# Kernel tuning notes

Hardware: AMD Instinct MI355X
Metric: run time of the kernel (lower is better)

Reference implementation:

```python
import jax, jax.numpy as jnp
import numpy as np

# Module constants (from init_kwargs)
MAP_BBOX = (-5.0, -5.0, 5.0, 5.0)  # h1, w1, h2, w2
V_BBOX = (0.0, 3.0)
MAP_RES = (64, 64)
V_RES = 8
XYZ_TO_H, XYZ_TO_W, XYZ_TO_V = 0, 1, 2
SCALE = 4
PCN_H = 64


def mish(x):
    return x * jnp.tanh(jax.nn.softplus(x))


def conv_d2(x, w):
    # 3x3 conv, dilation 2, padding 2, stride 1, no bias (NCHW / OIHW)
    return jax.lax.conv_general_dilated(
        x, w, window_strides=(1, 1), padding=((2, 2), (2, 2)),
        rhs_dilation=(2, 2), dimension_numbers=('NCHW', 'OIHW', 'NCHW'))


def maxpool3s2(x):
    # MaxPool2d(kernel=3, stride=2, padding=1); torch pads with -inf
    return jax.lax.reduce_window(
        x, -jnp.inf, jax.lax.max,
        window_dimensions=(1, 1, 3, 3), window_strides=(1, 1, 2, 2),
        padding=((0, 0), (0, 0), (1, 1), (1, 1)))


def setup_inputs() -> dict:
    key = jax.random.key(0)
    k1, k2, k3, k4, k5 = jax.random.split(key, 5)
    N, H, W = 64, 256, 256
    B = 8
    return {
        'rgb': jax.random.normal(k1, (N, 3, H, W), dtype=jnp.float32),
        'surf_xyz': jax.random.normal(k2, (N, 3, H, W), dtype=jnp.float32),
        'W1': jax.random.normal(k3, (PCN_H, 3, 3, 3), dtype=jnp.float32) * 0.1,
        'W2': jax.random.normal(k4, (PCN_H, PCN_H, 3, 3), dtype=jnp.float32) * 0.05,
        'index': jax.random.randint(k5, (N,), 0, B, dtype=jnp.int32),
        'batch_size': B,
    }


def reference(rgb, surf_xyz, W1, W2, index, batch_size):
    N, _, H, W = surf_xyz.shape
    s = SCALE
    Hs, Ws = H // s, W // s

    # avg_pool2d(rgb, 4)
    surf_rgb = rgb.reshape(N, 3, Hs, s, Ws, s).mean(axis=(3, 5))
    # subsampled xyz: surf_xyz[:, :, 2::4, 2::4]
    sxyz = surf_xyz[:, :, s // 2::s, s // 2::s]  # (N,3,Hs,Ws)
    _index = jnp.broadcast_to(index[:, None, None], (N, Hs, Ws))

    # rgb_conv_net: conv -> mish -> maxpool -> conv -> mish -> maxpool (dropout=0)
    feat = maxpool3s2(mish(conv_d2(rgb, W1)))
    feat = maxpool3s2(mish(conv_d2(feat, W2)))  # (N, h, Hs, Ws)

    # flatten  (valid_points is None path)
    hdim = feat.shape[1]
    flat_features = feat.transpose(0, 2, 3, 1).reshape(-1, hdim)   # (M, h)
    flat_xyz = sxyz.transpose(0, 2, 3, 1).reshape(-1, 3)           # (M, 3)
    flat_rgb = surf_rgb.transpose(0, 2, 3, 1).reshape(-1, 3)       # (M, 3)
    flat_index = _index.reshape(-1)                                # (M,)

    # coord_to_grid (float->int cast truncates toward zero, matching torch .long())
    map_h, map_w = MAP_RES
    h1, w1, h2, w2 = MAP_BBOX
    v1, v2 = V_BBOX
    hs = ((flat_xyz[:, XYZ_TO_H] - h1) * map_h / (h2 - h1)).astype(jnp.int32)
    ws = ((flat_xyz[:, XYZ_TO_W] - w1) * map_w / (w2 - w1)).astype(jnp.int32)
    vs = ((flat_xyz[:, XYZ_TO_V] - v1) * V_RES / (v2 - v1)).astype(jnp.int32)
    valid = ((hs >= 0) & (hs < map_h) & (ws >= 0) & (ws < map_w)
             & (vs >= 0) & (vs < V_RES))

    B, V = batch_size, V_RES
    P = B * V * map_h * map_w
    lin = ((flat_index * V + vs) * map_h + hs) * map_w + ws
    # route invalid points to a dummy segment that gets dropped
    lin_safe = jnp.where(valid, lin, P)

    sums = jax.ops.segment_sum(flat_features, lin_safe, num_segments=P + 1)[:P]
    rgbs = jax.ops.segment_sum(flat_rgb, lin_safe, num_segments=P + 1)[:P]
    counts = jax.ops.segment_sum(
        jnp.ones_like(lin_safe), lin_safe, num_segments=P + 1)[:P]

    feature_map = sums.reshape(B, V, map_h, map_w, hdim).transpose(0, 4, 1, 2, 3)
    rgb_map = rgbs.reshape(B, V, map_h, map_w, 3).transpose(0, 4, 1, 2, 3)
    feature_counts = counts.reshape(B, V, map_h, map_w)[:, None]
    return feature_map, feature_counts, rgb_map
```

## Files before the change

### kernel.cpp

```cpp
#include <hip/hip_runtime.h>
#include <hip/hip_bf16.h>
#include <math.h>

#define N_IMG 64
#define CH    64
#define F1_R  136
#define F1_C  136
#define F1_IMG_STRIDE ((size_t)F1_R * F1_C * 64)
#define F1_ROW_STRIDE (F1_C * 64)
#define FEAT1_BYTES ((size_t)N_IMG * F1_IMG_STRIDE * 2)

#define OUT_CNT_BASE 16777216
#define OUT_RGB_BASE 17039360

typedef short bf16x8 __attribute__((ext_vector_type(8)));
typedef float f32x4  __attribute__((ext_vector_type(4)));

__device__ __forceinline__ float fast_mish(float x) {
    float xc = fminf(x, 20.0f);
    float t  = __expf(xc);
    float n  = t * (t + 2.0f);
    float y  = x * n / (n + 2.0f);
    return (x > 20.0f) ? x : y;
}

__device__ __forceinline__ unsigned short f2bf(float f) {
    unsigned u = __float_as_uint(f);
    unsigned r = (u + 0x7FFFu + ((u >> 16) & 1u)) >> 16;
    return (unsigned short)r;
}

__global__ __launch_bounds__(256) void point_kernel(
    const float* __restrict__ rgb,
    const float* __restrict__ sxyz,
    const int*   __restrict__ index,
    float*       __restrict__ out,
    int*         __restrict__ lin_pt)
{
    int p = blockIdx.x * 256 + threadIdx.x;
    int n  = p >> 12;
    int r  = p & 4095;
    int hs = r >> 6;
    int ws = r & 63;

    int row = hs * 4 + 2, col = ws * 4 + 2;
    const float* sx = sxyz + (size_t)n * 3 * 65536;
    float X = sx[row * 256 + col];
    float Y = sx[65536 + row * 256 + col];
    float Z = sx[2 * 65536 + row * 256 + col];

    int hb = (int)(((X + 5.0f) * 64.0f) / 10.0f);
    int wb = (int)(((Y + 5.0f) * 64.0f) / 10.0f);
    int vb = (int)((Z * 8.0f) / 3.0f);
    bool valid = (hb >= 0) & (hb < 64) & (wb >= 0) & (wb < 64) & (vb >= 0) & (vb < 8);

    int b   = index[n];
    int lin = ((b * 8 + vb) * 64 + hb) * 64 + wb;
    lin_pt[p] = valid ? lin : -1;

    if (valid) {
        atomicAdd(out + OUT_CNT_BASE + lin, 1.0f);
        int rem = lin & 32767;
        #pragma unroll
        for (int c = 0; c < 3; c++) {
            const float* rg = rgb + (size_t)(n * 3 + c) * 65536;
            float s = 0.0f;
            #pragma unroll
            for (int i = 0; i < 4; i++)
                #pragma unroll
                for (int j = 0; j < 4; j++)
                    s += rg[(hs * 4 + i) * 256 + (ws * 4 + j)];
            atomicAdd(out + OUT_RGB_BASE + b * 98304 + c * 32768 + rem, s * 0.0625f);
        }
    }
}

__global__ __launch_bounds__(1024) void conv1_mfma_kernel(
    const float* __restrict__ rgb,
    const float* __restrict__ w1,
    __hip_bfloat16* __restrict__ feat1)
{
    int b2 = ((blockIdx.x & 7) << 9) + (blockIdx.x >> 3);
    const int n  = b2 >> 6;
    const int pr = b2 & 63;
    const int tid  = threadIdx.x;
    const int lane = tid & 63;
    const int w    = tid >> 6;

    __shared__ __align__(16) char smem[81920];
    unsigned short* wlds = (unsigned short*)smem;
    unsigned short* in_t = (unsigned short*)(smem + 4096);

    for (int i = tid; i < 2048; i += 1024) {
        int co = i >> 5, k = i & 31;
        wlds[i] = (k < 27) ? f2bf(w1[co * 27 + k]) : (unsigned short)0;
    }
    {
        const float* img = rgb + (size_t)n * 3 * 65536;
        for (int i = tid; i < 7144; i += 1024) {
            unsigned short v = 0;
            if (i < 7128) {
                int ci  = i / 2376;
                int rem = i - ci * 2376;
                int rr  = rem / 264;
                int cc  = rem - rr * 264;
                int gy  = 4 * pr - 3 + rr;
                int gx  = cc - 2;
                if (gy >= 0 && gy < 256 && gx >= 0 && gx < 256)
                    v = f2bf(img[ci * 65536 + gy * 256 + gx]);
            }
            in_t[i] = v;
        }
    }
    __syncthreads();

    int boff[8];
    #pragma unroll
    for (int j = 0; j < 8; j++) {
        int k = ((lane >> 4) << 3) + j;
        if (k < 27) {
            int ci = k / 9, t = k - 9 * ci, ky = t / 3, kx = t - 3 * ky;
            boff[j] = (ci * 2376 + 2 * ky * 264 + 2 * kx + (lane & 15)) * 2;
        } else {
            boff[j] = 7128 * 2;
        }
    }

    bf16x8 a[4];
    #pragma unroll
    for (int mt = 0; mt < 4; mt++)
        a[mt] = *reinterpret_cast<const bf16x8*>(
            wlds + (mt * 16 + (lane & 15)) * 32 + ((lane >> 4) << 3));

    f32x4 acc[5][4];
    #pragma unroll
    for (int tt = 0; tt < 5; tt++)
        #pragma unroll
        for (int mt = 0; mt < 4; mt++)
            acc[tt][mt] = (f32x4){0.f, 0.f, 0.f, 0.f};

    const char* in_b = (const char*)in_t;
    #pragma unroll
    for (int tt = 0; tt < 5; tt++) {
        int t5 = w * 5 + tt;
        int r  = t5 >> 4;
        int x0 = (t5 & 15) << 4;
        int base = (r * 264 + x0) * 2;
        unsigned short e[8];
        #pragma unroll
        for (int j = 0; j < 8; j++)
            e[j] = *reinterpret_cast<const unsigned short*>(in_b + base + boff[j]);
        bf16x8 b;
        #pragma unroll
        for (int j = 0; j < 8; j++) b[j] = (short)e[j];
        #pragma unroll
        for (int mt = 0; mt < 4; mt++)
            acc[tt][mt] = __builtin_amdgcn_mfma_f32_16x16x32_bf16(a[mt], b, acc[tt][mt], 0, 0, 0);
    }

    __syncthreads();

    unsigned short* pool = (unsigned short*)smem;
    const int ybase = 4 * pr - 1;

    #pragma unroll
    for (int p = 0; p < 2; p++) {
        #pragma unroll
        for (int tt = 0; tt < 5; tt++) {
            int t5 = w * 5 + tt;
            int r  = t5 >> 4;
            int x  = ((t5 & 15) << 4) + (lane & 15);
            bool dead = (ybase + r) < 0;
            #pragma unroll
            for (int m2 = 0; m2 < 2; m2++) {
                int mt  = p * 2 + m2;
                int col = m2 * 16 + ((lane >> 4) << 2);
                unsigned long long pk = 0;
                #pragma unroll
                for (int q = 0; q < 4; q++) {
                    float v = dead ? -INFINITY : fast_mish(acc[tt][mt][q]);
                    pk |= (unsigned long long)f2bf(v) << (16 * q);
                }
                int byte = (((r * 256 + x) * 32) + col) * 2;
                byte ^= (x & 7) << 4;
                *reinterpret_cast<unsigned long long*>((char*)pool + byte) = pk;
            }
        }
        __syncthreads();
        for (int i = tid; i < 8192; i += 1024) {
            int pp = i >> 12;
            int c  = (i >> 5) & 127;
            int cl = i & 31;
            float m = -INFINITY;
            #pragma unroll
            for (int dy = 0; dy < 3; dy++) {
                int lr = 2 * pp + dy;
                #pragma unroll
                for (int dx = 0; dx < 3; dx++) {
                    int x = 2 * c - 1 + dx;
                    if (x < 0) continue;
                    int byte = ((((lr * 256) + x) * 32) + cl) * 2;
                    byte ^= (x & 7) << 4;
                    unsigned short hv = *reinterpret_cast<const unsigned short*>((char*)pool + byte);
                    m = fmaxf(m, __uint_as_float((unsigned)hv << 16));
                }
            }
            unsigned short* dst = (unsigned short*)(feat1 + (size_t)n * F1_IMG_STRIDE
                + (size_t)(2 * pr + pp + 4) * F1_ROW_STRIDE + (size_t)(c + 4) * 64 + p * 32 + cl);
            *dst = f2bf(m);
        }
        __syncthreads();
    }
}

__global__ __launch_bounds__(640, 3) void conv2_mfma_kernel(
    const __hip_bfloat16* __restrict__ feat1,
    const float* __restrict__ w2,
    const int*   __restrict__ lin_pt,
    float*       __restrict__ out)
{
    int b2 = ((blockIdx.x & 7) << 8) + (blockIdx.x >> 3);
    const int n  = b2 >> 5;
    const int pr = b2 & 31;
    const int tid  = threadIdx.x;
    const int lane = tid & 63;
    const int w    = tid >> 6;
    const int lrow = w >> 1;
    const int chalf = w & 1;
    const int y = 4 * pr - 1 + lrow;

    __shared__ __align__(16) char smem[81920];

    for (int i = tid; i < 36864; i += 640) {
        int t  = i >> 12;
        int co = (i >> 6) & 63;
        int ci = i & 63;
        unsigned short h = f2bf(w2[(co * 64 + ci) * 9 + t]);
        int byte = ((((t << 6) + co) << 6) + ci) << 1;
        byte ^= (co & 7) << 4;
        *reinterpret_cast<unsigned short*>(smem + byte) = h;
    }
    __syncthreads();

    f32x4 acc[4][4];
    #pragma unroll
    for (int mt = 0; mt < 4; mt++)
        #pragma unroll
        for (int nt = 0; nt < 4; nt++)
            acc[mt][nt] = (f32x4){0.f, 0.f, 0.f, 0.f};

    const __hip_bfloat16* bbase = feat1 + (size_t)n * F1_IMG_STRIDE
        + ((size_t)(y + 2) * F1_C + (lane & 15) + chalf * 64 + 2) * 64
        + ((lane >> 4) << 3);

    #pragma unroll
    for (int ky = 0; ky < 3; ky++) {
        #pragma unroll
        for (int kx = 0; kx < 3; kx++) {
            const int t = ky * 3 + kx;
            #pragma unroll
            for (int s = 0; s < 2; s++) {
                bf16x8 a[4];
                #pragma unroll
                for (int mt = 0; mt < 4; mt++) {
                    int co = mt * 16 + (lane & 15);
                    int byte = ((((t << 6) + co) << 6) + (s << 5) + ((lane >> 4) << 3)) << 1;
                    byte ^= (co & 7) << 4;
                    a[mt] = *reinterpret_cast<const bf16x8*>(smem + byte);
                }
                const __hip_bfloat16* bp = bbase + (ky * 2 * F1_C + kx * 2) * 64 + s * 32;
                #pragma unroll
                for (int nt = 0; nt < 4; nt++) {
                    bf16x8 b = *reinterpret_cast<const bf16x8*>(bp + nt * 1024);
                    #pragma unroll
                    for (int mt = 0; mt < 4; mt++)
                        acc[mt][nt] = __builtin_amdgcn_mfma_f32_16x16x32_bf16(
                            a[mt], b, acc[mt][nt], 0, 0, 0);
                }
            }
        }
    }

    __syncthreads();

    const bool deadrow = (y < 0);
    #pragma unroll
    for (int nt = 0; nt < 4; nt++) {
        int col = chalf * 64 + nt * 16 + (lane & 15);
        #pragma unroll
        for (int mt = 0; mt < 4; mt++) {
            int co0 = mt * 16 + ((lane >> 4) << 2);
            unsigned long long pk = 0;
            #pragma unroll
            for (int r4 = 0; r4 < 4; r4++) {
                float v = deadrow ? -INFINITY : fast_mish(acc[mt][nt][r4]);
                pk |= (unsigned long long)f2bf(v) << (16 * r4);
            }
            int byte = ((((lrow * 128 + col) << 6) + co0) << 1);
            byte ^= (col & 7) << 4;
            *reinterpret_cast<unsigned long long*>(smem + byte) = pk;
        }
    }
    __syncthreads();

    const int pbase = (n << 12) + ((pr << 1) << 6);
    for (int i = tid; i < 8192; i += 640) {
        int pp = i >> 12;
        int c  = (i >> 6) & 63;
        int co = i & 63;
        float m = -INFINITY;
        #pragma unroll
        for (int dy = 0; dy < 3; dy++) {
            int lr = 2 * pp + dy;
            #pragma unroll
            for (int dx = 0; dx < 3; dx++) {
                int x = 2 * c - 1 + dx;
                if (x < 0 || x > 127) continue;
                int byte = ((((lr * 128 + x) << 6) + co) << 1) ^ ((x & 7) << 4);
                unsigned short hv = *reinterpret_cast<const unsigned short*>(smem + byte);
                m = fmaxf(m, __uint_as_float((unsigned)hv << 16));
            }
        }
        int lin = lin_pt[pbase + (pp << 6) + c];
        if (lin >= 0)
            atomicAdd(out + (size_t)(lin >> 15) * 2097152 + (size_t)co * 32768 + (lin & 32767), m);
    }
}

extern "C" void kernel_launch(void* const* d_in, const int* in_sizes, int n_in,
                              void* d_out, int out_size, void* d_ws, size_t ws_size,
                              hipStream_t stream)
{
    const float* rgb   = (const float*)d_in[0];
    const float* sxyz  = (const float*)d_in[1];
    const float* w1    = (const float*)d_in[2];
    const float* w2    = (const float*)d_in[3];
    const int*   index = (const int*)d_in[4];
    float* out = (float*)d_out;

    __hip_bfloat16* feat1 = (__hip_bfloat16*)d_ws;
    int* lin_pt = (int*)((char*)d_ws + FEAT1_BYTES);

    hipMemsetAsync(d_out, 0, (size_t)out_size * 4, stream);
    hipMemsetAsync(d_ws, 0, FEAT1_BYTES, stream);

    point_kernel<<<1024, 256, 0, stream>>>(rgb, sxyz, index, out, lin_pt);
    conv1_mfma_kernel<<<4096, 1024, 0, stream>>>(rgb, w1, feat1);
    conv2_mfma_kernel<<<2048, 640, 0, stream>>>(feat1, w2, lin_pt, out);
}
```

Baseline: 1.211 ms.

## Pre-convert conv2 weights to bf16 in global memory and halve conv2 LDS footprint

Adds a small kernel that converts W2 to bf16 once into workspace, so conv2 blocks no longer each convert and stage the full weight tensor in LDS. A-fragments are read directly from global/L2, and the mish+maxpool epilogue is split into two 32-channel passes so shared memory drops from 80 KB to 40 KB. The smaller LDS allows more resident blocks per CU and removes the per-block weight prologue. The cost is more global/L2 traffic for weight loads inside the MFMA loop, an extra sync, and one extra kernel launch.

```diff
diff --git a/kernel.cpp b/kernel.cpp
--- a/kernel.cpp
+++ b/kernel.cpp
@@ -9,6 +9,7 @@
 #define F1_IMG_STRIDE ((size_t)F1_R * F1_C * 64)
 #define F1_ROW_STRIDE (F1_C * 64)
 #define FEAT1_BYTES ((size_t)N_IMG * F1_IMG_STRIDE * 2)
+#define LINPT_BYTES (262144 * 4)
 
 #define OUT_CNT_BASE 16777216
 #define OUT_RGB_BASE 17039360
@@ -28,6 +29,18 @@
     unsigned u = __float_as_uint(f);
     unsigned r = (u + 0x7FFFu + ((u >> 16) & 1u)) >> 16;
     return (unsigned short)r;
+}
+
+__global__ __launch_bounds__(256) void w2cvt_kernel(
+    const float* __restrict__ w2, unsigned short* __restrict__ w2bf)
+{
+    int i = blockIdx.x * 256 + threadIdx.x;
+    if (i < 36864) {
+        int t  = i >> 12;
+        int co = (i >> 6) & 63;
+        int ci = i & 63;
+        w2bf[i] = f2bf(w2[(co * 64 + ci) * 9 + t]);
+    }
 }
 
 __global__ __launch_bounds__(256) void point_kernel(
@@ -213,9 +226,9 @@
     }
 }
 
-__global__ __launch_bounds__(640, 3) void conv2_mfma_kernel(
+__global__ __launch_bounds__(640) void conv2_mfma_kernel(
     const __hip_bfloat16* __restrict__ feat1,
-    const float* __restrict__ w2,
+    const unsigned short* __restrict__ w2bf,
     const int*   __restrict__ lin_pt,
     float*       __restrict__ out)
 {
@@ -229,18 +242,7 @@
     const int chalf = w & 1;
     const int y = 4 * pr - 1 + lrow;
 
-    __shared__ __align__(16) char smem[81920];
-
-    for (int i = tid; i < 36864; i += 640) {
-        int t  = i >> 12;
-        int co = (i >> 6) & 63;
-        int ci = i & 63;
-        unsigned short h = f2bf(w2[(co * 64 + ci) * 9 + t]);
-        int byte = ((((t << 6) + co) << 6) + ci) << 1;
-        byte ^= (co & 7) << 4;
-        *reinterpret_cast<unsigned short*>(smem + byte) = h;
-    }
-    __syncthreads();
+    __shared__ __align__(16) char smem[40960];
 
     f32x4 acc[4][4];
     #pragma unroll
@@ -252,6 +254,7 @@
     const __hip_bfloat16* bbase = feat1 + (size_t)n * F1_IMG_STRIDE
         + ((size_t)(y + 2) * F1_C + (lane & 15) + chalf * 64 + 2) * 64
         + ((lane >> 4) << 3);
+    const unsigned short* abase = w2bf + (size_t)(lane & 15) * 64 + ((lane >> 4) << 3);
 
     #pragma unroll
     for (int ky = 0; ky < 3; ky++) {
@@ -262,12 +265,9 @@
             for (int s = 0; s < 2; s++) {
                 bf16x8 a[4];
                 #pragma unroll
-                for (int mt = 0; mt < 4; mt++) {
-                    int co = mt * 16 + (lane & 15);
-                    int byte = ((((t << 6) + co) << 6) + (s << 5) + ((lane >> 4) << 3)) << 1;
-                    byte ^= (co & 7) << 4;
-                    a[mt] = *reinterpret_cast<const bf16x8*>(smem + byte);
-                }
+                for (int mt = 0; mt < 4; mt++)
+                    a[mt] = *reinterpret_cast<const bf16x8*>(
+                        abase + ((t * 64 + mt * 16) * 64) + s * 32);
                 const __hip_bfloat16* bp = bbase + (ky * 2 * F1_C + kx * 2) * 64 + s * 32;
                 #pragma unroll
                 for (int nt = 0; nt < 4; nt++) {
@@ -281,49 +281,53 @@
         }
     }
 
-    __syncthreads();
-
     const bool deadrow = (y < 0);
-    #pragma unroll
-    for (int nt = 0; nt < 4; nt++) {
-        int col = chalf * 64 + nt * 16 + (lane & 15);
-        #pragma unroll
-        for (int mt = 0; mt < 4; mt++) {
-            int co0 = mt * 16 + ((lane >> 4) << 2);
-            unsigned long long pk = 0;
-            #pragma unroll
-            for (int r4 = 0; r4 < 4; r4++) {
-                float v = deadrow ? -INFINITY : fast_mish(acc[mt][nt][r4]);
-                pk |= (unsigned long long)f2bf(v) << (16 * r4);
-            }
-            int byte = ((((lrow * 128 + col) << 6) + co0) << 1);
-            byte ^= (col & 7) << 4;
-            *reinterpret_cast<unsigned long long*>(smem + byte) = pk;
-        }
-    }
-    __syncthreads();
-
     const int pbase = (n << 12) + ((pr << 1) << 6);
-    for (int i = tid; i < 8192; i += 640) {
-        int pp = i >> 12;
-        int c  = (i >> 6) & 63;
-        int co = i & 63;
-        float m = -INFINITY;
-        #pragma unroll
-        for (int dy = 0; dy < 3; dy++) {
-            int lr = 2 * pp + dy;
-            #pragma unroll
-            for (int dx = 0; dx < 3; dx++) {
-                int x = 2 * c - 1 + dx;
-                if (x < 0 || x > 127) continue;
-                int byte = ((((lr * 128 + x) << 6) + co) << 1) ^ ((x & 7) << 4);
-                unsigned short hv = *reinterpret_cast<const unsigned short*>(smem + byte);
-                m = fmaxf(m, __uint_as_float((unsigned)hv << 16));
-            }
-        }
-        int lin = lin_pt[pbase + (pp << 6) + c];
-        if (lin >= 0)
-            atomicAdd(out + (size_t)(lin >> 15) * 2097152 + (size_t)co * 32768 + (lin & 32767), m);
+
+    #pragma unroll
+    for (int p = 0; p < 2; p++) {
+        if (p) __syncthreads();
+        #pragma unroll
+        for (int nt = 0; nt < 4; nt++) {
+            int col = chalf * 64 + nt * 16 + (lane & 15);
+            #pragma unroll
+            for (int m2 = 0; m2 < 2; m2++) {
+                int mt  = p * 2 + m2;
+                int cl0 = m2 * 16 + ((lane >> 4) << 2);
+                unsigned long long pk = 0;
+                #pragma unroll
+                for (int r4 = 0; r4 < 4; r4++) {
+                    float v = deadrow ? -INFINITY : fast_mish(acc[mt][nt][r4]);
+                    pk |= (unsigned long long)f2bf(v) << (16 * r4);
+                }
+                int byte = (((lrow * 128 + col) * 32) + cl0) * 2;
+                byte ^= (col & 7) << 4;
+                *reinterpret_cast<unsigned long long*>(smem + byte) = pk;
+            }
+        }
+        __syncthreads();
+        for (int i = tid; i < 4096; i += 640) {
+            int pp = i >> 11;
+            int c  = (i >> 5) & 63;
+            int cl = i & 31;
+            float m = -INFINITY;
+            #pragma unroll
+            for (int dy = 0; dy < 3; dy++) {
+                int lr = 2 * pp + dy;
+                #pragma unroll
+                for (int dx = 0; dx < 3; dx++) {
+                    int x = 2 * c - 1 + dx;
+                    if (x < 0 || x > 127) continue;
+                    int byte = ((((lr * 128 + x) * 32) + cl) * 2) ^ ((x & 7) << 4);
+                    unsigned short hv = *reinterpret_cast<const unsigned short*>(smem + byte);
+                    m = fmaxf(m, __uint_as_float((unsigned)hv << 16));
+                }
+            }
+            int lin = lin_pt[pbase + (pp << 6) + c];
+            if (lin >= 0)
+                atomicAdd(out + (size_t)(lin >> 15) * 2097152
+                              + (size_t)(p * 32 + cl) * 32768 + (lin & 32767), m);
+        }
     }
 }
 
@@ -340,11 +344,13 @@
 
     __hip_bfloat16* feat1 = (__hip_bfloat16*)d_ws;
     int* lin_pt = (int*)((char*)d_ws + FEAT1_BYTES);
+    unsigned short* w2bf = (unsigned short*)((char*)d_ws + FEAT1_BYTES + LINPT_BYTES);
 
     hipMemsetAsync(d_out, 0, (size_t)out_size * 4, stream);
     hipMemsetAsync(d_ws, 0, FEAT1_BYTES, stream);
 
+    w2cvt_kernel<<<144, 256, 0, stream>>>(w2, w2bf);
     point_kernel<<<1024, 256, 0, stream>>>(rgb, sxyz, index, out, lin_pt);
     conv1_mfma_kernel<<<4096, 1024, 0, stream>>>(rgb, w1, feat1);
-    conv2_mfma_kernel<<<2048, 640, 0, stream>>>(feat1, w2, lin_pt, out);
-}
+    conv2_mfma_kernel<<<2048, 640, 0, stream>>>(feat1, w2bf, lin_pt, out);
+}
```

New measurement: 1.287 ms. +6.4%, slower.
